# Performance work log

Measured on AMD Instinct MI355X. Metric: run time of the kernel, lower is better.

## Reference

```python
import jax, jax.numpy as jnp
import numpy as np

NUM_HEADS = 12
HEAD_DIM = 64
ROPE_THETA = 10000.0
WINDOW = 128  # local_attention: total window, +/- WINDOW//2 around each query
NEG_INF = jnp.finfo(jnp.float32).min


def _rotate_half(x):
    x1, x2 = jnp.split(x, 2, axis=-1)
    return jnp.concatenate([-x2, x1], axis=-1)


def _rope_cos_sin(position_ids, head_dim, theta):
    # position_ids: [B, S] int -> cos/sin: [B, S, head_dim]
    inv_freq = 1.0 / (theta ** (jnp.arange(0, head_dim, 2, dtype=jnp.float32) / head_dim))
    freqs = position_ids.astype(jnp.float32)[..., None] * inv_freq  # [B, S, hd/2]
    emb = jnp.concatenate([freqs, freqs], axis=-1)  # [B, S, hd]
    return jnp.cos(emb), jnp.sin(emb)


def setup_inputs() -> dict:
    key = jax.random.key(0)
    k1, k2, k3 = jax.random.split(key, 3)
    B, S, H = 4, 2048, 768
    hidden_states = jax.random.normal(k1, (B, S, H), dtype=jnp.float32)
    position_ids = jnp.broadcast_to(jnp.arange(S, dtype=jnp.int64), (B, S))
    Wqkv = jax.random.normal(k2, (3 * H, H), dtype=jnp.float32) * 0.02
    Wo = jax.random.normal(k3, (H, H), dtype=jnp.float32) * 0.02
    return {"hidden_states": hidden_states, "position_ids": position_ids, "Wqkv": Wqkv, "Wo": Wo}


def reference(hidden_states, position_ids, Wqkv, Wo):
    B, S, H = hidden_states.shape
    nh, hd = NUM_HEADS, HEAD_DIM
    # QKV projection (no bias, attention_bias=False)
    qkv = jnp.einsum("bsh,oh->bso", hidden_states, Wqkv)  # [B, S, 3H]
    qkv = qkv.reshape(B, S, 3, nh, hd)
    # torch: qkv.transpose(3,1).unbind(dim=2) -> q,k,v: [B, nh, S, hd]
    qkv = jnp.transpose(qkv, (0, 3, 2, 1, 4))
    query, key, value = qkv[:, :, 0], qkv[:, :, 1], qkv[:, :, 2]
    # RoPE (NeoX style, non-interleaved)
    cos, sin = _rope_cos_sin(position_ids, hd, ROPE_THETA)  # [B, S, hd]
    cos = cos[:, None]  # [B, 1, S, hd]
    sin = sin[:, None]
    query = query * cos + _rotate_half(query) * sin
    key = key * cos + _rotate_half(key) * sin
    # sliding-window additive mask: attend iff |i - j| <= WINDOW // 2
    idx = jnp.arange(S)
    in_window = jnp.abs(idx[:, None] - idx[None, :]) <= (WINDOW // 2)
    mask = jnp.where(in_window, 0.0, NEG_INF)[None, None]  # [1, 1, S, S]
    scale = hd ** (-0.5)
    scores = jnp.einsum("bhqd,bhkd->bhqk", query, key) * scale + mask
    attn = jax.nn.softmax(scores.astype(jnp.float32), axis=-1).astype(query.dtype)
    out = jnp.einsum("bhqk,bhkd->bhqd", attn, value)  # [B, nh, S, hd]
    out = jnp.transpose(out, (0, 2, 1, 3)).reshape(B, S, H)
    # output projection
    return jnp.einsum("bsh,oh->bso", out, Wo)
```

## Files before the change

### kernel.cpp

```cpp
#include <hip/hip_runtime.h>
#include <hip/hip_bf16.h>

#define Bn 4
#define Sn 2048
#define Hn 768
#define NHn 12
#define Mn (Bn*Sn)
#define QKVN 2304

typedef unsigned short u16;
typedef unsigned int u32;
typedef __attribute__((ext_vector_type(8))) short short8;
typedef __attribute__((ext_vector_type(4))) float f32x4;

typedef __attribute__((address_space(1))) const u32 g_u32;
typedef __attribute__((address_space(3))) u32 l_u32;

__device__ __forceinline__ void gll16(const void* g, void* l) {
    __builtin_amdgcn_global_load_lds((g_u32*)g, (l_u32*)l, 16, 0, 0);
}

__device__ __forceinline__ u16 f2bf(float f) {
    u32 x = __float_as_uint(f);
    x += 0x7fffu + ((x >> 16) & 1u);
    return (u16)(x >> 16);
}
__device__ __forceinline__ float bf2f(u16 u) {
    return __uint_as_float(((u32)u) << 16);
}

__global__ __launch_bounds__(256) void cast3_k(const float* __restrict__ hs,
                                               const float* __restrict__ wqkv,
                                               const float* __restrict__ wo,
                                               u16* __restrict__ hs_b,
                                               u16* __restrict__ wqkv_b,
                                               u16* __restrict__ wo_b) {
    int i = blockIdx.x * 256 + threadIdx.x;
    const float* s; u16* d; int off;
    if (i < 1572864)      { s = hs;   d = hs_b;   off = i; }
    else if (i < 2015232) { s = wqkv; d = wqkv_b; off = i - 1572864; }
    else if (i < 2162688) { s = wo;   d = wo_b;   off = i - 2015232; }
    else return;
    float4 v = ((const float4*)s)[off];
    ushort4 o;
    o.x = f2bf(v.x); o.y = f2bf(v.y); o.z = f2bf(v.z); o.w = f2bf(v.w);
    ((ushort4*)d)[off] = o;
}

__global__ __launch_bounds__(256) void tab_k(const int* __restrict__ pos_ids,
                                             float2* __restrict__ tab) {
    int idx = blockIdx.x * 256 + threadIdx.x;
    int d2 = idx & 31, row = idx >> 5;
    float invf = exp2f((float)d2 * -0.4152410119f);
    float fr = (float)pos_ids[row] * invf;
    float sn, cs;
    sincosf(fr, &sn, &cs);
    tab[idx] = make_float2(cs, sn);
}

template <int BM, int BN, typename OUT, bool ROPE>
__global__ __launch_bounds__(256, 4) void gemm_bt(const u16* __restrict__ A,
                                                  const u16* __restrict__ Bw,
                                                  OUT* __restrict__ C,
                                                  const float2* __restrict__ tab,
                                                  int N, int K) {
    constexpr int WM = BM / 2, WN = BN / 2;
    constexpr int MR = WM / 16, NR = WN / 16;
    static_assert(!ROPE || NR == 4, "ROPE fusion assumes wave spans one 64-head");
    __shared__ __align__(16) u16 As[BM * 64];
    __shared__ __align__(16) u16 Bs[BN * 64];
    const int t = threadIdx.x;
    const int wid = t >> 6, lane = t & 63;
    const int wr = wid >> 1, wc = wid & 1;
    const long m0 = (long)blockIdx.x * BM;
    const long n0 = (long)blockIdx.y * BN;
    const int lr = lane & 15, g = lane >> 4;

    f32x4 acc[MR][NR] = {};

    for (int kt = 0; kt < K; kt += 64) {
        #pragma unroll
        for (int ss = 0; ss < BM / 32; ++ss) {
            int s = t + ss * 256;
            int row = s >> 3, gg = s & 7;
            int col8 = (gg ^ (row & 7)) * 8;
            gll16(A + (m0 + row) * K + kt + col8, (char*)As + s * 16);
        }
        #pragma unroll
        for (int ss = 0; ss < BN / 32; ++ss) {
            int s = t + ss * 256;
            int row = s >> 3, gg = s & 7;
            int col8 = (gg ^ (row & 7)) * 8;
            gll16(Bw + (n0 + row) * K + kt + col8, (char*)Bs + s * 16);
        }
        __syncthreads();
        #pragma unroll
        for (int kk2 = 0; kk2 < 2; ++kk2) {
            const int slot = kk2 * 4 + g;
            short8 bfr[NR];
            #pragma unroll
            for (int nt = 0; nt < NR; ++nt) {
                int row = wc * WN + nt * 16 + lr;
                bfr[nt] = *(const short8*)((const char*)Bs + row * 128 +
                                           ((slot ^ (row & 7)) << 4));
            }
            #pragma unroll
            for (int mt = 0; mt < MR; ++mt) {
                int row = wr * WM + mt * 16 + lr;
                short8 af = *(const short8*)((const char*)As + row * 128 +
                                             ((slot ^ (row & 7)) << 4));
                #pragma unroll
                for (int nt = 0; nt < NR; ++nt)
                    acc[mt][nt] = __builtin_amdgcn_mfma_f32_16x16x32_bf16(
                        af, bfr[nt], acc[mt][nt], 0, 0, 0);
            }
        }
        __syncthreads();
    }

    if constexpr (ROPE) {
        if ((n0 + wc * WN) < 1536) {
            #pragma unroll
            for (int mt = 0; mt < MR; ++mt)
                #pragma unroll
                for (int r = 0; r < 4; ++r) {
                    long row = m0 + wr * WM + mt * 16 + g * 4 + r;
                    const float2* tr = tab + row * 32;
                    #pragma unroll
                    for (int ntp = 0; ntp < 2; ++ntp) {
                        float2 cssn = tr[ntp * 16 + lr];
                        float x1 = acc[mt][ntp][r], x2 = acc[mt][ntp + 2][r];
                        acc[mt][ntp][r]     = x1 * cssn.x - x2 * cssn.y;
                        acc[mt][ntp + 2][r] = x2 * cssn.x + x1 * cssn.y;
                    }
                }
        }
    }

    #pragma unroll
    for (int mt = 0; mt < MR; ++mt)
        #pragma unroll
        for (int nt = 0; nt < NR; ++nt)
            #pragma unroll
            for (int r = 0; r < 4; ++r) {
                long row = m0 + wr * WM + mt * 16 + g * 4 + r;
                long col = n0 + wc * WN + nt * 16 + lr;
                float v = acc[mt][nt][r];
                if constexpr (sizeof(OUT) == 2) C[row * N + col] = (OUT)f2bf(v);
                else                            C[row * N + col] = v;
            }
}

__global__ __launch_bounds__(256) void attn_k(const u16* __restrict__ qkv,
                                              u16* __restrict__ outb) {
    const int qt = blockIdx.x, bh = blockIdx.y;
    const int b = bh / NHn, h = bh % NHn;
    const int q0 = qt * 64, kv0 = q0 - 64;
    const int t = threadIdx.x, wid = t >> 6, lane = t & 63;
    const int lr = lane & 15, g = lane >> 4;

    __shared__ __align__(16) char smem[58368];
    u16* Qs = (u16*)smem;
    u16* Ks = (u16*)(smem + 8192);
    u16* Vt = (u16*)(smem + 32768);

    const size_t rowbase = (size_t)b * Sn;

    #pragma unroll
    for (int ss = 0; ss < 2; ++ss) {
        int s = t + ss * 256;
        int row = s >> 3, gg = s & 7;
        int col8 = (gg ^ (row & 7)) * 8;
        gll16(qkv + (rowbase + q0 + row) * QKVN + h * 64 + col8, (char*)Qs + s * 16);
    }
    #pragma unroll
    for (int ss = 0; ss < 6; ++ss) {
        int s = t + ss * 256;
        int row = s >> 3, gg = s & 7;
        int kk = kv0 + row;
        kk = kk < 0 ? 0 : (kk > Sn - 1 ? Sn - 1 : kk);
        int col8 = (gg ^ (row & 7)) * 8;
        gll16(qkv + (rowbase + kk) * QKVN + 768 + h * 64 + col8, (char*)Ks + s * 16);
    }
    #pragma unroll
    for (int ss = 0; ss < 6; ++ss) {
        int s = t + ss * 256;
        int krow = s >> 3, gg = s & 7;
        int kk = kv0 + krow;
        kk = kk < 0 ? 0 : (kk > Sn - 1 ? Sn - 1 : kk);
        short8 v = *(const short8*)(qkv + (rowbase + kk) * QKVN + 1536 + h * 64 + gg * 8);
        #pragma unroll
        for (int j = 0; j < 8; ++j) Vt[(gg * 8 + j) * 200 + krow] = (u16)v[j];
    }
    __syncthreads();

    f32x4 sacc[12] = {};
    #pragma unroll
    for (int kk2 = 0; kk2 < 2; ++kk2) {
        int qrow = wid * 16 + lr;
        int slot = kk2 * 4 + g;
        short8 qf = *(const short8*)((const char*)Qs + qrow * 128 + ((slot ^ (qrow & 7)) << 4));
        #pragma unroll
        for (int tl = 0; tl < 12; ++tl) {
            int krow = tl * 16 + lr;
            short8 kf = *(const short8*)((const char*)Ks + krow * 128 + ((slot ^ (krow & 7)) << 4));
            sacc[tl] = __builtin_amdgcn_mfma_f32_16x16x32_bf16(qf, kf, sacc[tl], 0, 0, 0);
        }
    }

    float p[12][4];
    float lsum[4];
    #pragma unroll
    for (int r = 0; r < 4; ++r) {
        int qq = q0 + wid * 16 + g * 4 + r;
        float mx = -3.0e38f;
        #pragma unroll
        for (int tl = 0; tl < 12; ++tl) {
            int kq = kv0 + tl * 16 + lr;
            float sc = sacc[tl][r] * 0.125f;
            int dqk = qq - kq;
            bool valid = (kq >= 0) && (kq < Sn) && (dqk <= 64) && (dqk >= -64);
            sc = valid ? sc : -3.0e38f;
            p[tl][r] = sc;
            mx = fmaxf(mx, sc);
        }
        #pragma unroll
        for (int mk = 1; mk < 16; mk <<= 1) mx = fmaxf(mx, __shfl_xor(mx, mk, 16));
        float sum = 0.f;
        #pragma unroll
        for (int tl = 0; tl < 12; ++tl) {
            float e = __expf(p[tl][r] - mx);
            p[tl][r] = e;
            sum += e;
        }
        #pragma unroll
        for (int mk = 1; mk < 16; mk <<= 1) sum += __shfl_xor(sum, mk, 16);
        lsum[r] = sum;
    }

    __syncthreads();

    u16* Pw = (u16*)(smem + wid * 6400);
    #pragma unroll
    for (int tl = 0; tl < 12; ++tl)
        #pragma unroll
        for (int r = 0; r < 4; ++r)
            Pw[(g * 4 + r) * 200 + tl * 16 + lr] = f2bf(p[tl][r]);

    f32x4 oacc[4] = {};
    #pragma unroll
    for (int ks = 0; ks < 6; ++ks) {
        short8 pf = *(const short8*)((const char*)Pw + lr * 400 + (ks * 32 + g * 8) * 2);
        #pragma unroll
        for (int dt = 0; dt < 4; ++dt) {
            short8 vf = *(const short8*)((const char*)Vt + (dt * 16 + lr) * 400 + (ks * 32 + g * 8) * 2);
            oacc[dt] = __builtin_amdgcn_mfma_f32_16x16x32_bf16(pf, vf, oacc[dt], 0, 0, 0);
        }
    }

    #pragma unroll
    for (int dt = 0; dt < 4; ++dt)
        #pragma unroll
        for (int r = 0; r < 4; ++r) {
            int row = q0 + wid * 16 + g * 4 + r;
            float v = oacc[dt][r] / lsum[r];
            outb[(rowbase + row) * Hn + h * 64 + dt * 16 + lr] = f2bf(v);
        }
}

extern "C" void kernel_launch(void* const* d_in, const int* in_sizes, int n_in,
                              void* d_out, int out_size, void* d_ws, size_t ws_size,
                              hipStream_t stream) {
    const float* hs   = (const float*)d_in[0];
    const int*   pos  = (const int*)d_in[1];
    const float* wqkv = (const float*)d_in[2];
    const float* wo   = (const float*)d_in[3];
    float* out = (float*)d_out;
    char* ws = (char*)d_ws;

    u16* hs_b   = (u16*)(ws);
    u16* wqkv_b = (u16*)(ws + 12582912);
    u16* wo_b   = (u16*)(ws + 16121856);
    u16* qkv    = (u16*)(ws + 17301504);
    u16* attn   = (u16*)(ws + 55050240);
    float2* tab = (float2*)(ws + 55050240);

    cast3_k<<<8448, 256, 0, stream>>>(hs, wqkv, wo, hs_b, wqkv_b, wo_b);
    tab_k<<<1024, 256, 0, stream>>>(pos, tab);

    gemm_bt<128, 128, u16, true><<<dim3(64, 18), 256, 0, stream>>>(
        hs_b, wqkv_b, qkv, tab, 2304, 768);

    attn_k<<<dim3(32, 48), 256, 0, stream>>>(qkv, attn);

    gemm_bt<128, 64, float, false><<<dim3(64, 12), 256, 0, stream>>>(
        attn, wo_b, out, nullptr, 768, 768);
}
```

Measured before the change: 98.88 us.

## Double-buffer GEMM LDS tiles and merge cast and RoPE table kernels

The GEMM now keeps two LDS buffers for the A and B tiles and issues the global-to-LDS loads for the next K tile before computing on the current one, so load latency can overlap the MFMA work. The cast kernel and the RoPE sin/cos table kernel are merged into one launch to save a kernel launch. Doubling LDS per block may lower occupancy (the 128x128 tile now needs 64KB). With only one barrier per iteration, the async loads into the other buffer are issued right after that barrier and may not be guaranteed complete before they are read, which is a possible race.

```diff
diff --git a/kernel.cpp b/kernel.cpp
--- a/kernel.cpp
+++ b/kernel.cpp
@@ -29,13 +29,25 @@
     return __uint_as_float(((u32)u) << 16);
 }
 
-__global__ __launch_bounds__(256) void cast3_k(const float* __restrict__ hs,
-                                               const float* __restrict__ wqkv,
-                                               const float* __restrict__ wo,
-                                               u16* __restrict__ hs_b,
-                                               u16* __restrict__ wqkv_b,
-                                               u16* __restrict__ wo_b) {
+__global__ __launch_bounds__(256) void prep_k(const float* __restrict__ hs,
+                                              const float* __restrict__ wqkv,
+                                              const float* __restrict__ wo,
+                                              const int* __restrict__ pos_ids,
+                                              u16* __restrict__ hs_b,
+                                              u16* __restrict__ wqkv_b,
+                                              u16* __restrict__ wo_b,
+                                              float2* __restrict__ tab) {
     int i = blockIdx.x * 256 + threadIdx.x;
+    if (i < 262144) {
+        int d2 = i & 31, row = i >> 5;
+        float invf = exp2f((float)d2 * -0.4152410119f);
+        float fr = (float)pos_ids[row] * invf;
+        float sn, cs;
+        sincosf(fr, &sn, &cs);
+        tab[i] = make_float2(cs, sn);
+        return;
+    }
+    i -= 262144;
     const float* s; u16* d; int off;
     if (i < 1572864)      { s = hs;   d = hs_b;   off = i; }
     else if (i < 2015232) { s = wqkv; d = wqkv_b; off = i - 1572864; }
@@ -47,17 +59,6 @@
     ((ushort4*)d)[off] = o;
 }
 
-__global__ __launch_bounds__(256) void tab_k(const int* __restrict__ pos_ids,
-                                             float2* __restrict__ tab) {
-    int idx = blockIdx.x * 256 + threadIdx.x;
-    int d2 = idx & 31, row = idx >> 5;
-    float invf = exp2f((float)d2 * -0.4152410119f);
-    float fr = (float)pos_ids[row] * invf;
-    float sn, cs;
-    sincosf(fr, &sn, &cs);
-    tab[idx] = make_float2(cs, sn);
-}
-
 template <int BM, int BN, typename OUT, bool ROPE>
 __global__ __launch_bounds__(256, 4) void gemm_bt(const u16* __restrict__ A,
                                                   const u16* __restrict__ Bw,
@@ -67,8 +68,8 @@
     constexpr int WM = BM / 2, WN = BN / 2;
     constexpr int MR = WM / 16, NR = WN / 16;
     static_assert(!ROPE || NR == 4, "ROPE fusion assumes wave spans one 64-head");
-    __shared__ __align__(16) u16 As[BM * 64];
-    __shared__ __align__(16) u16 Bs[BN * 64];
+    __shared__ __align__(16) u16 As[2][BM * 64];
+    __shared__ __align__(16) u16 Bs[2][BN * 64];
     const int t = threadIdx.x;
     const int wid = t >> 6, lane = t & 63;
     const int wr = wid >> 1, wc = wid & 1;
@@ -78,22 +79,31 @@
 
     f32x4 acc[MR][NR] = {};
 
-    for (int kt = 0; kt < K; kt += 64) {
+    auto stage = [&](int buf, int kt) {
         #pragma unroll
         for (int ss = 0; ss < BM / 32; ++ss) {
             int s = t + ss * 256;
             int row = s >> 3, gg = s & 7;
             int col8 = (gg ^ (row & 7)) * 8;
-            gll16(A + (m0 + row) * K + kt + col8, (char*)As + s * 16);
+            gll16(A + (m0 + row) * K + kt + col8, (char*)As[buf] + s * 16);
         }
         #pragma unroll
         for (int ss = 0; ss < BN / 32; ++ss) {
             int s = t + ss * 256;
             int row = s >> 3, gg = s & 7;
             int col8 = (gg ^ (row & 7)) * 8;
-            gll16(Bw + (n0 + row) * K + kt + col8, (char*)Bs + s * 16);
-        }
-        __syncthreads();
+            gll16(Bw + (n0 + row) * K + kt + col8, (char*)Bs[buf] + s * 16);
+        }
+    };
+
+    const int NT = K / 64;
+    stage(0, 0);
+    __syncthreads();
+    int cur = 0;
+    for (int it = 0; it < NT; ++it) {
+        if (it + 1 < NT) stage(cur ^ 1, (it + 1) * 64);
+        const u16* Ab = As[cur];
+        const u16* Bb = Bs[cur];
         #pragma unroll
         for (int kk2 = 0; kk2 < 2; ++kk2) {
             const int slot = kk2 * 4 + g;
@@ -101,13 +111,13 @@
             #pragma unroll
             for (int nt = 0; nt < NR; ++nt) {
                 int row = wc * WN + nt * 16 + lr;
-                bfr[nt] = *(const short8*)((const char*)Bs + row * 128 +
+                bfr[nt] = *(const short8*)((const char*)Bb + row * 128 +
                                            ((slot ^ (row & 7)) << 4));
             }
             #pragma unroll
             for (int mt = 0; mt < MR; ++mt) {
                 int row = wr * WM + mt * 16 + lr;
-                short8 af = *(const short8*)((const char*)As + row * 128 +
+                short8 af = *(const short8*)((const char*)Ab + row * 128 +
                                              ((slot ^ (row & 7)) << 4));
                 #pragma unroll
                 for (int nt = 0; nt < NR; ++nt)
@@ -116,6 +126,7 @@
             }
         }
         __syncthreads();
+        cur ^= 1;
     }
 
     if constexpr (ROPE) {
@@ -285,8 +296,7 @@
     u16* attn   = (u16*)(ws + 55050240);
     float2* tab = (float2*)(ws + 55050240);
 
-    cast3_k<<<8448, 256, 0, stream>>>(hs, wqkv, wo, hs_b, wqkv_b, wo_b);
-    tab_k<<<1024, 256, 0, stream>>>(pos, tab);
+    prep_k<<<9472, 256, 0, stream>>>(hs, wqkv, wo, pos, hs_b, wqkv_b, wo_b, tab);
 
     gemm_bt<128, 128, u16, true><<<dim3(64, 18), 256, 0, stream>>>(
         hs_b, wqkv_b, qkv, tab, 2304, 768);
```

After: 106.8 us. 1.08x slower.

## Add 4-stage pipelined 256x256 QKV GEMM and merge cast and RoPE-table kernels

Applied to the files above, without the earlier changes.

Replaces the QKV projection GEMM with a 512-thread kernel that uses 256x256 tiles, a 4-slot LDS ring of K=32 stages filled by global_load_lds, interleaved barriers with s_setprio around the MFMA bursts, and a swizzled block order. The goal is to hide global-load latency and get more reuse per tile than the old 128x128 single-buffered loop. The cast and RoPE-table kernels are also merged into one launch to save a launch. The trade-off is only 288 blocks with heavy LDS and register use, which may leave CUs poorly filled or cause a tail.

```diff
diff --git a/kernel.cpp b/kernel.cpp
--- a/kernel.cpp
+++ b/kernel.cpp
@@ -29,13 +29,25 @@
     return __uint_as_float(((u32)u) << 16);
 }
 
-__global__ __launch_bounds__(256) void cast3_k(const float* __restrict__ hs,
-                                               const float* __restrict__ wqkv,
-                                               const float* __restrict__ wo,
-                                               u16* __restrict__ hs_b,
-                                               u16* __restrict__ wqkv_b,
-                                               u16* __restrict__ wo_b) {
+__global__ __launch_bounds__(256) void prep_k(const float* __restrict__ hs,
+                                              const float* __restrict__ wqkv,
+                                              const float* __restrict__ wo,
+                                              const int* __restrict__ pos_ids,
+                                              u16* __restrict__ hs_b,
+                                              u16* __restrict__ wqkv_b,
+                                              u16* __restrict__ wo_b,
+                                              float2* __restrict__ tab) {
     int i = blockIdx.x * 256 + threadIdx.x;
+    if (i < 262144) {
+        int d2 = i & 31, row = i >> 5;
+        float invf = exp2f((float)d2 * -0.4152410119f);
+        float fr = (float)pos_ids[row] * invf;
+        float sn, cs;
+        sincosf(fr, &sn, &cs);
+        tab[i] = make_float2(cs, sn);
+        return;
+    }
+    i -= 262144;
     const float* s; u16* d; int off;
     if (i < 1572864)      { s = hs;   d = hs_b;   off = i; }
     else if (i < 2015232) { s = wqkv; d = wqkv_b; off = i - 1572864; }
@@ -47,26 +59,143 @@
     ((ushort4*)d)[off] = o;
 }
 
-__global__ __launch_bounds__(256) void tab_k(const int* __restrict__ pos_ids,
-                                             float2* __restrict__ tab) {
-    int idx = blockIdx.x * 256 + threadIdx.x;
-    int d2 = idx & 31, row = idx >> 5;
-    float invf = exp2f((float)d2 * -0.4152410119f);
-    float fr = (float)pos_ids[row] * invf;
-    float sn, cs;
-    sincosf(fr, &sn, &cs);
-    tab[idx] = make_float2(cs, sn);
-}
-
-template <int BM, int BN, typename OUT, bool ROPE>
+#define KWAIT(N) do { \
+    asm volatile("s_waitcnt vmcnt(" #N ")" ::: "memory"); \
+    __builtin_amdgcn_s_barrier(); \
+    __builtin_amdgcn_sched_barrier(0); \
+} while (0)
+
+__global__ __launch_bounds__(512, 2) void gemm_pipe(const u16* __restrict__ A,
+                                                    const u16* __restrict__ Bw,
+                                                    u16* __restrict__ C,
+                                                    const float2* __restrict__ tab) {
+    constexpr int K = 768, N = QKVN, NT = K / 32;
+    __shared__ __align__(16) u16 As[4][256 * 32];
+    __shared__ __align__(16) u16 Bs[4][256 * 32];
+    const int t = threadIdx.x;
+    const int wid = t >> 6, lane = t & 63;
+    const int wm = wid >> 2, wn = wid & 3;
+    const int lr = lane & 15, g = lane >> 4;
+
+    int bid = blockIdx.x;
+    int sw = (bid & 7) * 36 + (bid >> 3);
+    const long m0 = (long)(sw / 9) * 256;
+    const long n0 = (long)(sw % 9) * 256;
+
+    f32x4 acc[8][4] = {};
+
+    auto stageA = [&](int slot, int kt) {
+        #pragma unroll
+        for (int j = 0; j < 2; ++j) {
+            int idx = t + j * 512;
+            int row = idx >> 2, gg = idx & 3;
+            int col8 = (gg ^ ((row >> 1) & 3)) * 8;
+            gll16(A + (m0 + row) * K + kt * 32 + col8, (char*)As[slot] + idx * 16);
+        }
+    };
+    auto stageB = [&](int slot, int kt) {
+        #pragma unroll
+        for (int j = 0; j < 2; ++j) {
+            int idx = t + j * 512;
+            int row = idx >> 2, gg = idx & 3;
+            int col8 = (gg ^ ((row >> 1) & 3)) * 8;
+            gll16(Bw + (n0 + row) * K + kt * 32 + col8, (char*)Bs[slot] + idx * 16);
+        }
+    };
+
+    auto computeTile = [&](int slot, int kstage) {
+        const u16* Ab = As[slot];
+        const u16* Bb = Bs[slot];
+        short8 bf_[4], af_[4];
+        #pragma unroll
+        for (int nf = 0; nf < 4; ++nf) {
+            int row = wn * 64 + nf * 16 + lr;
+            bf_[nf] = *(const short8*)((const char*)Bb + row * 64 +
+                                       ((g ^ ((row >> 1) & 3)) << 4));
+        }
+        #pragma unroll
+        for (int mf = 0; mf < 4; ++mf) {
+            int row = wm * 128 + mf * 16 + lr;
+            af_[mf] = *(const short8*)((const char*)Ab + row * 64 +
+                                       ((g ^ ((row >> 1) & 3)) << 4));
+        }
+        if (kstage >= 0) stageA(kstage & 3, kstage);
+        __builtin_amdgcn_s_barrier();
+        __builtin_amdgcn_s_setprio(1);
+        #pragma unroll
+        for (int mf = 0; mf < 4; ++mf)
+            #pragma unroll
+            for (int nf = 0; nf < 4; ++nf)
+                acc[mf][nf] = __builtin_amdgcn_mfma_f32_16x16x32_bf16(
+                    af_[mf], bf_[nf], acc[mf][nf], 0, 0, 0);
+        __builtin_amdgcn_s_setprio(0);
+        __builtin_amdgcn_s_barrier();
+        #pragma unroll
+        for (int mf = 0; mf < 4; ++mf) {
+            int row = wm * 128 + 64 + mf * 16 + lr;
+            af_[mf] = *(const short8*)((const char*)Ab + row * 64 +
+                                       ((g ^ ((row >> 1) & 3)) << 4));
+        }
+        if (kstage >= 0) stageB(kstage & 3, kstage);
+        __builtin_amdgcn_s_barrier();
+        __builtin_amdgcn_s_setprio(1);
+        #pragma unroll
+        for (int mf = 0; mf < 4; ++mf)
+            #pragma unroll
+            for (int nf = 0; nf < 4; ++nf)
+                acc[mf + 4][nf] = __builtin_amdgcn_mfma_f32_16x16x32_bf16(
+                    af_[mf], bf_[nf], acc[mf + 4][nf], 0, 0, 0);
+        __builtin_amdgcn_s_setprio(0);
+    };
+
+    stageA(0, 0); stageB(0, 0);
+    stageA(1, 1); stageB(1, 1);
+    stageA(2, 2); stageB(2, 2);
+
+    for (int it = 0; it <= NT - 4; ++it) {
+        KWAIT(8);
+        computeTile(it & 3, it + 3);
+    }
+    KWAIT(8); computeTile((NT - 3) & 3, -1);
+    KWAIT(4); computeTile((NT - 2) & 3, -1);
+    KWAIT(0); computeTile((NT - 1) & 3, -1);
+
+    if ((n0 + wn * 64) < 1536) {
+        #pragma unroll
+        for (int mf = 0; mf < 8; ++mf)
+            #pragma unroll
+            for (int r = 0; r < 4; ++r) {
+                long row = m0 + wm * 128 + mf * 16 + g * 4 + r;
+                const float2* tr = tab + row * 32;
+                #pragma unroll
+                for (int ntp = 0; ntp < 2; ++ntp) {
+                    float2 cssn = tr[ntp * 16 + lr];
+                    float x1 = acc[mf][ntp][r], x2 = acc[mf][ntp + 2][r];
+                    acc[mf][ntp][r]     = x1 * cssn.x - x2 * cssn.y;
+                    acc[mf][ntp + 2][r] = x2 * cssn.x + x1 * cssn.y;
+                }
+            }
+    }
+
+    #pragma unroll
+    for (int mf = 0; mf < 8; ++mf)
+        #pragma unroll
+        for (int nf = 0; nf < 4; ++nf)
+            #pragma unroll
+            for (int r = 0; r < 4; ++r) {
+                long row = m0 + wm * 128 + mf * 16 + g * 4 + r;
+                long col = n0 + wn * 64 + nf * 16 + lr;
+                C[row * N + col] = f2bf(acc[mf][nf][r]);
+            }
+}
+
+template <int BM, int BN, typename OUT>
 __global__ __launch_bounds__(256, 4) void gemm_bt(const u16* __restrict__ A,
                                                   const u16* __restrict__ Bw,
                                                   OUT* __restrict__ C,
-                                                  const float2* __restrict__ tab,
                                                   int N, int K) {
     constexpr int WM = BM / 2, WN = BN / 2;
     constexpr int MR = WM / 16, NR = WN / 16;
-    static_assert(!ROPE || NR == 4, "ROPE fusion assumes wave spans one 64-head");
     __shared__ __align__(16) u16 As[BM * 64];
     __shared__ __align__(16) u16 Bs[BN * 64];
     const int t = threadIdx.x;
@@ -118,25 +247,6 @@
         __syncthreads();
     }
 
-    if constexpr (ROPE) {
-        if ((n0 + wc * WN) < 1536) {
-            #pragma unroll
-            for (int mt = 0; mt < MR; ++mt)
-                #pragma unroll
-                for (int r = 0; r < 4; ++r) {
-                    long row = m0 + wr * WM + mt * 16 + g * 4 + r;
-                    const float2* tr = tab + row * 32;
-                    #pragma unroll
-                    for (int ntp = 0; ntp < 2; ++ntp) {
-                        float2 cssn = tr[ntp * 16 + lr];
-                        float x1 = acc[mt][ntp][r], x2 = acc[mt][ntp + 2][r];
-                        acc[mt][ntp][r]     = x1 * cssn.x - x2 * cssn.y;
-                        acc[mt][ntp + 2][r] = x2 * cssn.x + x1 * cssn.y;
-                    }
-                }
-        }
-    }
-
     #pragma unroll
     for (int mt = 0; mt < MR; ++mt)
         #pragma unroll
@@ -285,14 +395,12 @@
     u16* attn   = (u16*)(ws + 55050240);
     float2* tab = (float2*)(ws + 55050240);
 
-    cast3_k<<<8448, 256, 0, stream>>>(hs, wqkv, wo, hs_b, wqkv_b, wo_b);
-    tab_k<<<1024, 256, 0, stream>>>(pos, tab);
-
-    gemm_bt<128, 128, u16, true><<<dim3(64, 18), 256, 0, stream>>>(
-        hs_b, wqkv_b, qkv, tab, 2304, 768);
+    prep_k<<<9472, 256, 0, stream>>>(hs, wqkv, wo, pos, hs_b, wqkv_b, wo_b, tab);
+
+    gemm_pipe<<<288, 512, 0, stream>>>(hs_b, wqkv_b, qkv, tab);
 
     attn_k<<<dim3(32, 48), 256, 0, stream>>>(qkv, attn);
 
-    gemm_bt<128, 64, float, false><<<dim3(64, 12), 256, 0, stream>>>(
-        attn, wo_b, out, nullptr, 768, 768);
-}
+    gemm_bt<128, 64, float><<<dim3(64, 12), 256, 0, stream>>>(
+        attn, wo_b, out, 768, 768);
+}
```

After: 122.7 us. 24.1% more time.
